# Performance work log

Measured on AMD Instinct MI355X. Metric: run time of the kernel, lower is better.

## Reference

```python
import jax, jax.numpy as jnp
import numpy as np

B, T_ENC, T_DEC = 32, 512, 32
ENC = DEC = EMB = ATT = OUT = 256
VOCAB = 32000
CHUNK = 8
SOS = 1


def _energy(enc, h, W, V, b, vv, g, vb, r):
    # enc: [B,T,ENC], h: [B,DEC] -> [B,T]
    t = jnp.tanh(enc @ W.T + (h @ V.T)[:, None, :] + b)           # [B,T,ATT]
    w_eff = (g[0] / jnp.linalg.norm(vv)) * vv                      # weight-normed v
    return t @ w_eff + vb[0] + r[0]


def _excl_cumprod(x):
    # exclusive safe cumprod along axis 1: [1, x0, x0*x1, ...]
    logs = jnp.cumsum(jnp.log(jnp.clip(x, 1e-10, 1.0)), axis=1)
    logs = jnp.concatenate([jnp.zeros_like(logs[:, :1]), logs[:, :-1]], axis=1)
    return jnp.exp(logs)


def _moving_sum(x, back, forward):
    # sliding-window sum over axis 1, window [j-back, j+forward]
    T = x.shape[1]
    w = back + forward + 1
    xp = jnp.pad(x, ((0, 0), (back, forward)))
    c = jnp.cumsum(xp, axis=1)
    c = jnp.concatenate([jnp.zeros_like(c[:, :1]), c], axis=1)
    return c[:, w:w + T] - c[:, :T]


def _chunkwise_beta(alpha, u, w):
    u = u - jnp.max(u, axis=1, keepdims=True)
    eu = jnp.exp(u)
    denom = jnp.clip(_moving_sum(eu, w - 1, 0), 1e-10, None)
    return eu * _moving_sum(alpha / denom, 0, w - 1)


def setup_inputs():
    key = jax.random.key(0)
    ks = jax.random.split(key, 20)
    s = 0.05
    rn = lambda k, shp: jax.random.normal(k, shp, jnp.float32) * s
    return {
        'encoder_outputs': jax.random.normal(ks[0], (B, T_ENC, ENC), jnp.float32),
        'decoder_inputs': jax.random.randint(ks[1], (B, T_DEC), 0, VOCAB),
        'h0': jax.random.normal(ks[2], (B, DEC), jnp.float32),
        'noise': jax.random.normal(ks[3], (T_DEC, B, T_ENC), jnp.float32),
        'emb': rn(ks[4], (VOCAB, EMB)),
        'W_ih': rn(ks[5], (DEC, EMB)), 'b_ih': jnp.zeros((DEC,), jnp.float32),
        'W_hh': rn(ks[6], (DEC, DEC)), 'b_hh': jnp.zeros((DEC,), jnp.float32),
        'Wm': rn(ks[7], (ATT, ENC)), 'Vm': rn(ks[8], (ATT, DEC)),
        'bm': rn(ks[9], (ATT,)), 'vvm': jax.random.normal(ks[10], (ATT,), jnp.float32),
        'gm': jnp.full((1,), (1.0 / ATT) ** 0.5, jnp.float32),
        'vbm': jnp.zeros((1,), jnp.float32), 'rm': jnp.full((1,), -4.0, jnp.float32),
        'Wc': rn(ks[11], (ATT, ENC)), 'Vc': rn(ks[12], (ATT, DEC)),
        'bc': rn(ks[13], (ATT,)), 'vvc': jax.random.normal(ks[14], (ATT,), jnp.float32),
        'gc': jnp.full((1,), (1.0 / ATT) ** 0.5, jnp.float32),
        'vbc': jnp.zeros((1,), jnp.float32), 'rc': jnp.full((1,), -4.0, jnp.float32),
        'W_comb': rn(ks[15], (OUT, ENC + DEC)),
        'W_proj': rn(ks[16], (VOCAB, OUT)), 'b_proj': jnp.zeros((VOCAB,), jnp.float32),
    }


def reference(encoder_outputs, decoder_inputs, h0, noise, emb,
              W_ih, b_ih, W_hh, b_hh,
              Wm, Vm, bm, vvm, gm, vbm, rm,
              Wc, Vc, bc, vvc, gc, vbc, rc,
              W_comb, W_proj, b_proj):
    batch = encoder_outputs.shape[0]
    alpha0 = jnp.zeros((batch, encoder_outputs.shape[1]), encoder_outputs.dtype).at[:, 0].set(1.0)
    x0 = jnp.full((batch,), SOS, dtype=decoder_inputs.dtype)

    def step(carry, xs):
        x_tok, h, alpha = carry
        noise_t, next_tok = xs
        x = emb[x_tok]                                             # embedding lookup
        h = jnp.tanh(x @ W_ih.T + b_ih + h @ W_hh.T + b_hh)        # RNNCell (tanh)
        e_m = _energy(encoder_outputs, h, Wm, Vm, bm, vvm, gm, vbm, rm)
        p = jax.nn.sigmoid(e_m + noise_t)
        cp = _excl_cumprod(1.0 - p)
        alpha = p * cp * jnp.cumsum(alpha / jnp.clip(cp, 1e-10, 1.0), axis=1)
        e_c = _energy(encoder_outputs, h, Wc, Vc, bc, vvc, gc, vbc, rc)
        beta = _chunkwise_beta(alpha, e_c, CHUNK)
        context = jnp.einsum('bt,bte->be', beta, encoder_outputs)
        attn = jnp.tanh(jnp.concatenate([context, h], axis=1) @ W_comb.T)
        logit = attn @ W_proj.T + b_proj
        return (next_tok, h, alpha), logit

    xs = (noise, decoder_inputs.T)
    _, logits = jax.lax.scan(step, (x0, h0, alpha0), xs)           # [T_dec,B,V]
    return jnp.transpose(logits, (1, 0, 2))                        # [B,T_dec,V]
```

## Files before the change

### kernel.cpp

```cpp
#include <hip/hip_runtime.h>
#include <cstddef>

#define B 32
#define T_ENC 512
#define T_DEC 32
#define E 256
#define VOCAB 32000
#define SOS 1

typedef __attribute__((ext_vector_type(8))) short short8;
typedef __attribute__((ext_vector_type(4))) float floatx4;

static const size_t OFF_ENCW   = 0;
static const size_t OFF_WEFFM  = OFF_ENCW + (size_t)B * T_ENC * 2 * E;
static const size_t OFF_WEFFC  = OFF_WEFFM + E;
static const size_t OFF_BSUM   = OFF_WEFFC + E;
static const size_t OFF_XIH    = OFF_BSUM + E;
static const size_t OFF_WHHT   = OFF_XIH + (size_t)T_DEC * B * E;
static const size_t OFF_VMT    = OFF_WHHT + (size_t)E * E;
static const size_t OFF_VCT    = OFF_VMT + (size_t)E * E;
static const size_t OFF_WCOMBT = OFF_VCT + (size_t)E * E;
static const size_t OFF_ATTNB  = OFF_WCOMBT + (size_t)2 * E * E;
static const size_t OFF_WPBF   = OFF_ATTNB + (size_t)T_DEC * B * E / 2;

static const size_t OUT_EMBX  = 0;
static const size_t OUT_BETA  = 262144;
static const size_t OUT_ACOMB = 786432;
static const size_t OUT_HALL  = 1310720;
static const size_t OUT_HV    = 1572864;
static const size_t OUT_PE    = 2097152;
static const size_t OUT_VMC   = 3145728;
static const size_t OUT_ZERO  = 3276800;
static const size_t OUT_WHI   = 3277312;
static const size_t OUT_WLO   = 3342848;
static const size_t OUT_B512  = 3408384;

__device__ __forceinline__ float ftanh(float x) {
  float ax = __builtin_fabsf(x);
  float e  = __expf(-2.f * ax);
  float r  = (1.f - e) * __builtin_amdgcn_rcpf(1.f + e);
  return __builtin_copysignf(r, x);
}

__device__ __forceinline__ float fsigmoid(float z) {
  return __builtin_amdgcn_rcpf(1.f + __expf(-z));
}

__device__ __forceinline__ float wredmax(float s) {
  s = fmaxf(s, __shfl_xor(s, 1, 64));  s = fmaxf(s, __shfl_xor(s, 2, 64));
  s = fmaxf(s, __shfl_xor(s, 4, 64));  s = fmaxf(s, __shfl_xor(s, 8, 64));
  s = fmaxf(s, __shfl_xor(s, 16, 64)); s = fmaxf(s, __shfl_xor(s, 32, 64));
  return s;
}

__device__ __forceinline__ unsigned short f2bf(float f) {
  unsigned int u = __float_as_uint(f);
  u = (u + 0x7fffu + ((u >> 16) & 1u)) >> 16;
  return (unsigned short)u;
}

__device__ __forceinline__ float bf2f(unsigned short h) {
  return __uint_as_float((unsigned int)h << 16);
}

__device__ __forceinline__ float wexcl(float tot, int lane) {
  float v = tot;
#pragma unroll
  for (int off = 1; off < 64; off <<= 1) {
    float y = __shfl_up(v, off, 64);
    if (lane >= off) v += y;
  }
  return v - tot;
}

__device__ __forceinline__ float dot4_wtanh(float4 s2a, float4 s2b, float4 w4) {
  float e, num, acc;
  e = __expf(s2a.x + s2b.x); num = __builtin_fmaf(-e, w4.x, w4.x);
  acc = num * __builtin_amdgcn_rcpf(1.f + e);
  e = __expf(s2a.y + s2b.y); num = __builtin_fmaf(-e, w4.y, w4.y);
  acc = __builtin_fmaf(num, __builtin_amdgcn_rcpf(1.f + e), acc);
  e = __expf(s2a.z + s2b.z); num = __builtin_fmaf(-e, w4.z, w4.z);
  acc = __builtin_fmaf(num, __builtin_amdgcn_rcpf(1.f + e), acc);
  e = __expf(s2a.w + s2b.w); num = __builtin_fmaf(-e, w4.w, w4.w);
  acc = __builtin_fmaf(num, __builtin_amdgcn_rcpf(1.f + e), acc);
  return acc;
}

__device__ __forceinline__ float4 scalem2(float4 v) {
  float4 r; r.x = -2.f * v.x; r.y = -2.f * v.y; r.z = -2.f * v.z; r.w = -2.f * v.w;
  return r;
}

__global__ __launch_bounds__(256) void prep_misc(
    const float* __restrict__ vvm, const float* __restrict__ gm, float* __restrict__ w_effm,
    const float* __restrict__ vvc, const float* __restrict__ gc, float* __restrict__ w_effc,
    const float* __restrict__ b_ih, const float* __restrict__ b_hh, float* __restrict__ bsum,
    const float* __restrict__ bm, const float* __restrict__ bc, float* __restrict__ bias512,
    const float* __restrict__ Vm, const float* __restrict__ Vc,
    float* __restrict__ Vmc, float* __restrict__ zero512,
    const float* __restrict__ Wm, const float* __restrict__ Wc,
    unsigned short* __restrict__ Whi, unsigned short* __restrict__ Wlo)
{
  __shared__ float red[256];
  const int blk = blockIdx.x, tid = threadIdx.x;
  if (blk < 2) {
    const float* vv = blk ? vvc : vvm;
    const float* g  = blk ? gc  : gm;
    float* out      = blk ? w_effc : w_effm;
    float v = vv[tid];
    red[tid] = v * v;
    __syncthreads();
    for (int off = 128; off > 0; off >>= 1) {
      if (tid < off) red[tid] += red[tid + off];
      __syncthreads();
    }
    float norm = sqrtf(red[0]);
    out[tid] = (g[0] / norm) * v;
  } else if (blk == 2) {
    bsum[tid] = b_ih[tid] + b_hh[tid];
    bias512[tid]       = bm[tid];
    bias512[256 + tid] = bc[tid];
    zero512[tid] = 0.f;
    zero512[256 + tid] = 0.f;
  } else if (blk < 131) {
    int i = (blk - 3) * 1024 + tid * 4;
    float4 v = (i < E * E) ? *(const float4*)(Vm + i) : *(const float4*)(Vc + i - E * E);
    *(float4*)(Vmc + i) = v;
  } else {
    int i = (blk - 131) * 1024 + tid * 4;
    float4 v = (i < E * E) ? *(const float4*)(Wm + i) : *(const float4*)(Wc + i - E * E);
    ushort4 h, l;
    h.x = f2bf(v.x); l.x = f2bf(v.x - bf2f(h.x));
    h.y = f2bf(v.y); l.y = f2bf(v.y - bf2f(h.y));
    h.z = f2bf(v.z); l.z = f2bf(v.z - bf2f(h.z));
    h.w = f2bf(v.w); l.w = f2bf(v.w - bf2f(h.w));
    *(ushort4*)(Whi + i) = h;
    *(ushort4*)(Wlo + i) = l;
  }
}

__global__ __launch_bounds__(256) void transpose2(
    const float* __restrict__ W_hh, float* __restrict__ W_hhT,
    const float* __restrict__ W_comb, float* __restrict__ W_combT)
{
  __shared__ float tl[32][33];
  const int blk = blockIdx.x;
  const float* in; float* out; int C, bx, by;
  if (blk < 64) { in = W_hh;   out = W_hhT;   C = 256; bx = blk & 7;  by = blk >> 3; }
  else { int k = blk - 64; in = W_comb; out = W_combT; C = 512; bx = k & 15; by = k >> 4; }
  const int R = 256;
  const int tx = threadIdx.x & 31, ty = threadIdx.x >> 5;
  const int c0 = bx * 32, r0 = by * 32;
#pragma unroll
  for (int k = 0; k < 4; k++)
    tl[ty + 8 * k][tx] = in[(size_t)(r0 + ty + 8 * k) * C + c0 + tx];
  __syncthreads();
#pragma unroll
  for (int k = 0; k < 4; k++)
    out[(size_t)(c0 + ty + 8 * k) * R + r0 + tx] = tl[tx][ty + 8 * k];
}

__global__ __launch_bounds__(256) void gather_emb(
    const int* __restrict__ dec, const float* __restrict__ emb, float* __restrict__ embX)
{
  int r = blockIdx.x, d = threadIdx.x;
  int s = r >> 5, b = r & 31;
  int tok = (s == 0) ? SOS : dec[b * T_DEC + s - 1];
  embX[(size_t)r * E + d] = emb[(size_t)tok * E + d];
}

__global__ __launch_bounds__(256) void cvt_bf16(
    const float* __restrict__ src, unsigned short* __restrict__ dst)
{
  size_t i = ((size_t)blockIdx.x * 256 + threadIdx.x) * 4;
  float4 v = *(const float4*)(src + i);
  ushort4 o;
  o.x = f2bf(v.x); o.y = f2bf(v.y); o.z = f2bf(v.z); o.w = f2bf(v.w);
  *(ushort4*)(dst + i) = o;
}

__global__ __launch_bounds__(256) void gemm_xwt(
    const float* __restrict__ A, const float* __restrict__ W,
    const float* __restrict__ bias, float* __restrict__ Y,
    int M, int N, int K)
{
  __shared__ float As[64][68];
  __shared__ float Ws[64][68];
  const int tid = threadIdx.x;
  const int tx = tid & 15, ty = tid >> 4;
  const int row0 = blockIdx.y * 64, col0 = blockIdx.x * 64;
  float acc[4][4];
#pragma unroll
  for (int i = 0; i < 4; i++)
#pragma unroll
    for (int j = 0; j < 4; j++) acc[i][j] = 0.f;

  for (int k0 = 0; k0 < K; k0 += 64) {
#pragma unroll
    for (int s = 0; s < 4; s++) {
      int i = (s << 4) + ty;
      int j = tx << 2;
      float4 av = *(const float4*)(A + (size_t)(row0 + i) * K + k0 + j);
      As[j][i] = av.x; As[j + 1][i] = av.y; As[j + 2][i] = av.z; As[j + 3][i] = av.w;
      float4 wv = *(const float4*)(W + (size_t)(col0 + i) * K + k0 + j);
      Ws[j][i] = wv.x; Ws[j + 1][i] = wv.y; Ws[j + 2][i] = wv.z; Ws[j + 3][i] = wv.w;
    }
    __syncthreads();
#pragma unroll
    for (int kk = 0; kk < 64; kk++) {
      const float4 af = *(const float4*)&As[kk][ty << 2];
      const float4 bf = *(const float4*)&Ws[kk][tx << 2];
      acc[0][0] += af.x * bf.x; acc[0][1] += af.x * bf.y; acc[0][2] += af.x * bf.z; acc[0][3] += af.x * bf.w;
      acc[1][0] += af.y * bf.x; acc[1][1] += af.y * bf.y; acc[1][2] += af.y * bf.z; acc[1][3] += af.y * bf.w;
      acc[2][0] += af.z * bf.x; acc[2][1] += af.z * bf.y; acc[2][2] += af.z * bf.z; acc[2][3] += af.z * bf.w;
      acc[3][0] += af.w * bf.x; acc[3][1] += af.w * bf.y; acc[3][2] += af.w * bf.z; acc[3][3] += af.w * bf.w;
    }
    __syncthreads();
  }
  const float4 bv = *(const float4*)(bias + col0 + (tx << 2));
#pragma unroll
  for (int i = 0; i < 4; i++) {
    float4 o;
    o.x = acc[i][0] + bv.x; o.y = acc[i][1] + bv.y;
    o.z = acc[i][2] + bv.z; o.w = acc[i][3] + bv.w;
    *(float4*)(Y + (size_t)(row0 + (ty << 2) + i) * N + col0 + (tx << 2)) = o;
  }
}

__global__ __launch_bounds__(256) void enc_mfma(
    const float* __restrict__ A,
    const unsigned short* __restrict__ Whi, const unsigned short* __restrict__ Wlo,
    const float* __restrict__ bias512, float* __restrict__ Y)
{
  __shared__ unsigned short a_hi[64][264];
  __shared__ unsigned short a_lo[64][264];
  const int tid = threadIdx.x;
  const int row0 = blockIdx.x * 64;
#pragma unroll
  for (int u = 0; u < 16; ++u) {
    int f = tid + (u << 8);
    int r = f >> 6, c = (f & 63) << 2;
    float4 v = *(const float4*)(A + (size_t)(row0 + r) * E + c);
    ushort4 h, l;
    h.x = f2bf(v.x); l.x = f2bf(v.x - bf2f(h.x));
    h.y = f2bf(v.y); l.y = f2bf(v.y - bf2f(h.y));
    h.z = f2bf(v.z); l.z = f2bf(v.z - bf2f(h.z));
    h.w = f2bf(v.w); l.w = f2bf(v.w - bf2f(h.w));
    *(ushort4*)&a_hi[r][c] = h;
    *(ushort4*)&a_lo[r][c] = l;
  }
  __syncthreads();
  const int lane = tid & 63, w = tid >> 6;
  const int m = lane & 15, q = lane >> 4;
  const int colbase = w << 7;
#pragma unroll
  for (int cp = 0; cp < 4; ++cp) {
    const int c0 = colbase + (cp << 5);
    floatx4 acc[4][2] = {};
    for (int k0 = 0; k0 < E; k0 += 32) {
      const size_t w0 = (size_t)(c0 + m) * E + (q << 3) + k0;
      const size_t w1 = (size_t)(c0 + 16 + m) * E + (q << 3) + k0;
      short8 bh0 = *(const short8*)(Whi + w0);
      short8 bl0 = *(const short8*)(Wlo + w0);
      short8 bh1 = *(const short8*)(Whi + w1);
      short8 bl1 = *(const short8*)(Wlo + w1);
#pragma unroll
      for (int rg = 0; rg < 4; ++rg) {
        short8 ah = *(const short8*)&a_hi[(rg << 4) + m][(q << 3) + k0];
        short8 al = *(const short8*)&a_lo[(rg << 4) + m][(q << 3) + k0];
        acc[rg][0] = __builtin_amdgcn_mfma_f32_16x16x32_bf16(ah, bh0, acc[rg][0], 0, 0, 0);
        acc[rg][0] = __builtin_amdgcn_mfma_f32_16x16x32_bf16(al, bh0, acc[rg][0], 0, 0, 0);
        acc[rg][0] = __builtin_amdgcn_mfma_f32_16x16x32_bf16(ah, bl0, acc[rg][0], 0, 0, 0);
        acc[rg][0] = __builtin_amdgcn_mfma_f32_16x16x32_bf16(al, bl0, acc[rg][0], 0, 0, 0);
        acc[rg][1] = __builtin_amdgcn_mfma_f32_16x16x32_bf16(ah, bh1, acc[rg][1], 0, 0, 0);
        acc[rg][1] = __builtin_amdgcn_mfma_f32_16x16x32_bf16(al, bh1, acc[rg][1], 0, 0, 0);
        acc[rg][1] = __builtin_amdgcn_mfma_f32_16x16x32_bf16(ah, bl1, acc[rg][1], 0, 0, 0);
        acc[rg][1] = __builtin_amdgcn_mfma_f32_16x16x32_bf16(al, bl1, acc[rg][1], 0, 0, 0);
      }
    }
    const float bia0 = bias512[c0 + m], bia1 = bias512[c0 + 16 + m];
#pragma unroll
    for (int rg = 0; rg < 4; ++rg)
#pragma unroll
      for (int r = 0; r < 4; ++r) {
        const size_t row = row0 + (rg << 4) + (q << 2) + r;
        Y[row * (2 * E) + c0 + m]      = acc[rg][0][r] + bia0;
        Y[row * (2 * E) + c0 + 16 + m] = acc[rg][1][r] + bia1;
      }
  }
}

__global__ __launch_bounds__(1024) void hchain_kernel(
    const float* __restrict__ Xih, const float* __restrict__ W_hhT,
    const float* __restrict__ h0,
    float* __restrict__ A_comb, float* __restrict__ h_all)
{
  __shared__ float h_s[E];
  __shared__ float red[1024];
  const int b = blockIdx.x, tid = threadIdx.x;
  const int c = tid >> 8, d = tid & 255, k0 = c * 64;
  float wreg[64];
#pragma unroll
  for (int j = 0; j < 64; ++j) wreg[j] = W_hhT[(size_t)(k0 + j) * E + d];
  if (tid < E) h_s[tid] = h0[(size_t)b * E + tid];
  __syncthreads();
  for (int s = 0; s < T_DEC; ++s) {
    float acc = 0.f;
#pragma unroll
    for (int j = 0; j < 64; j += 4) {
      float4 hh = *(const float4*)&h_s[k0 + j];
      acc += hh.x * wreg[j] + hh.y * wreg[j + 1] + hh.z * wreg[j + 2] + hh.w * wreg[j + 3];
    }
    red[tid] = acc;
    __syncthreads();
    if (tid < E) {
      float v = red[tid] + red[256 + tid] + red[512 + tid] + red[768 + tid]
              + Xih[((size_t)s * B + b) * E + tid];
      float hh = ftanh(v);
      h_s[tid] = hh;
      A_comb[((size_t)(b * T_DEC + s)) * (2 * E) + E + tid] = hh;
      h_all[((size_t)(b * T_DEC + s)) * E + tid] = hh;
    }
    __syncthreads();
  }
}

__global__ __launch_bounds__(512) void energy_kernel(
    const float* __restrict__ encW, const float* __restrict__ g_hv,
    const float* __restrict__ w_effm, const float* __restrict__ w_effc,
    const float* __restrict__ vbm, const float* __restrict__ rmp,
    const float* __restrict__ vbc, const float* __restrict__ rcp_,
    float* __restrict__ g_pe)
{
  __shared__ float hv_s[16 * 512];
  const int b = blockIdx.x, t0 = blockIdx.y << 5, s0 = blockIdx.z << 4;
  const int tid = threadIdx.x, lane = tid & 63, w = tid >> 6;
  const float* hvb = g_hv + ((size_t)(b * T_DEC + s0)) * 512;
  for (int i = tid * 4; i < 16 * 512; i += 2048) {
    float4 v = *(const float4*)(hvb + i);
    *(float4*)&hv_s[i] = scalem2(v);
  }
  __syncthreads();

  const float embias = vbm[0] + rmp[0];
  const float ecbias = vbc[0] + rcp_[0];
  const float bias_l = ((lane >> 2) & 1) ? ecbias : embias;
  const float4 wm4 = *(const float4*)(w_effm + lane * 4);
  const float4 wc4 = *(const float4*)(w_effc + lane * 4);
  const int t = t0 + (w << 2);
  const size_t rb = ((size_t)(b * T_ENC + t)) * 512 + lane * 4;
  const float4 em0 = scalem2(*(const float4*)(encW + rb));
  const float4 em1 = scalem2(*(const float4*)(encW + rb + 512));
  const float4 em2 = scalem2(*(const float4*)(encW + rb + 1024));
  const float4 em3 = scalem2(*(const float4*)(encW + rb + 1536));
  const float4 ec0 = scalem2(*(const float4*)(encW + rb + 256));
  const float4 ec1 = scalem2(*(const float4*)(encW + rb + 768));
  const float4 ec2 = scalem2(*(const float4*)(encW + rb + 1280));
  const float4 ec3 = scalem2(*(const float4*)(encW + rb + 1792));

  const bool sb0 = lane & 1, sb1 = lane & 2, sb2 = lane & 4;
  const int myr = lane >> 3;
  float pv0 = 0.f, pv1 = 0.f;

  for (int sl = 0; sl < 16; ++sl) {
    const float4 hm4 = *(const float4*)&hv_s[(sl << 9) + lane * 4];
    const float4 hc4 = *(const float4*)&hv_s[(sl << 9) + 256 + lane * 4];
    float v0 = dot4_wtanh(em0, hm4, wm4);
    float v1 = dot4_wtanh(em1, hm4, wm4);
    float v2 = dot4_wtanh(em2, hm4, wm4);
    float v3 = dot4_wtanh(em3, hm4, wm4);
    float v4 = dot4_wtanh(ec0, hc4, wc4);
    float v5 = dot4_wtanh(ec1, hc4, wc4);
    float v6 = dot4_wtanh(ec2, hc4, wc4);
    float v7 = dot4_wtanh(ec3, hc4, wc4);
    float k0_ = sb0 ? v1 : v0, s0_ = sb0 ? v0 : v1; k0_ += __shfl_xor(s0_, 1, 64);
    float k1_ = sb0 ? v3 : v2, s1_ = sb0 ? v2 : v3; k1_ += __shfl_xor(s1_, 1, 64);
    float k2_ = sb0 ? v5 : v4, s2_ = sb0 ? v4 : v5; k2_ += __shfl_xor(s2_, 1, 64);
    float k3_ = sb0 ? v7 : v6, s3_ = sb0 ? v6 : v7; k3_ += __shfl_xor(s3_, 1, 64);
    float kA = sb1 ? k1_ : k0_, sA = sb1 ? k0_ : k1_; kA += __shfl_xor(sA, 2, 64);
    float kB = sb1 ? k3_ : k2_, sB = sb1 ? k2_ : k3_; kB += __shfl_xor(sB, 2, 64);
    float dd = sb2 ? kB : kA, sD = sb2 ? kA : kB; dd += __shfl_xor(sD, 4, 64);
    dd += __shfl_xor(dd, 8, 64);
    dd += __shfl_xor(dd, 16, 64);
    dd += __shfl_xor(dd, 32, 64);
    float val = dd + bias_l;
    if ((sl & 7) == myr) {
      if (sl & 8) pv1 = val; else pv0 = val;
    }
  }
  const int row_l = lane & 3, type = (lane >> 2) & 1;
  const int tS = t + row_l;
  const int col = type * 32 + s0 + myr;
  g_pe[((size_t)((b << 6) + col)) * 512 + tS]     = pv0;
  g_pe[((size_t)((b << 6) + col + 8)) * 512 + tS] = pv1;
}

__global__ __launch_bounds__(64) void scan_kernel(
    const float* __restrict__ g_pe, const float* __restrict__ noise,
    float* __restrict__ beta_all)
{
  const int b = blockIdx.x, lane = threadIdx.x;
  const float* pe = g_pe + ((size_t)b << 15);
  float alpha[8];
#pragma unroll
  for (int i = 0; i < 8; ++i) alpha[i] = 0.f;
  if (lane == 0) alpha[0] = 1.f;

  for (int s = 0; s < T_DEC; ++s) {
    const float* nrow = noise + ((size_t)s * B + b) * T_ENC + lane * 8;
    float4 n0 = *(const float4*)nrow;
    float4 n1 = *(const float4*)(nrow + 4);
    float nz[8] = {n0.x, n0.y, n0.z, n0.w, n1.x, n1.y, n1.z, n1.w};
    const float* psm = pe + (size_t)s * 512 + lane * 8;
    const float* pec = pe + (size_t)(32 + s) * 512 + lane * 8;
    float4 m0 = *(const float4*)psm;
    float4 m1 = *(const float4*)(psm + 4);
    float4 e0 = *(const float4*)pec;
    float4 e1 = *(const float4*)(pec + 4);
    float smv[8] = {m0.x, m0.y, m0.z, m0.w, m1.x, m1.y, m1.z, m1.w};
    float ec[8]  = {e0.x, e0.y, e0.z, e0.w, e1.x, e1.y, e1.z, e1.w};
    float p[8];
#pragma unroll
    for (int i = 0; i < 8; ++i) p[i] = fsigmoid(smv[i] + nz[i]);
    float lgv[8], lci[8], run = 0.f;
#pragma unroll
    for (int i = 0; i < 8; ++i) {
      float omp = fminf(fmaxf(1.f - p[i], 1e-10f), 1.f);
      lgv[i] = __logf(omp);
      run += lgv[i];
      lci[i] = run;
    }
    float ex1 = wexcl(run, lane);
    float cp[8], ao[8];
#pragma unroll
    for (int i = 0; i < 8; ++i) {
      float incl = lci[i] + ex1;
      cp[i] = __expf(incl - lgv[i]);
      float cpc = fminf(fmaxf(cp[i], 1e-10f), 1.f);
      ao[i] = alpha[i] * __builtin_amdgcn_rcpf(cpc);
    }
    float run2 = 0.f, lc2[8];
#pragma unroll
    for (int i = 0; i < 8; ++i) { run2 += ao[i]; lc2[i] = run2; }
    float ex2 = wexcl(run2, lane);
    float alpha_new[8];
#pragma unroll
    for (int i = 0; i < 8; ++i) alpha_new[i] = p[i] * cp[i] * (lc2[i] + ex2);
    float mloc = ec[0];
#pragma unroll
    for (int i = 1; i < 8; ++i) mloc = fmaxf(mloc, ec[i]);
    float mx = wredmax(mloc);
    float eu[8];
#pragma unroll
    for (int i = 0; i < 8; ++i) eu[i] = __expf(ec[i] - mx);
    float run3 = 0.f, c1[8];
#pragma unroll
    for (int i = 0; i < 8; ++i) { run3 += eu[i]; c1[i] = run3; }
    float ex3 = wexcl(run3, lane);
#pragma unroll
    for (int i = 0; i < 8; ++i) c1[i] += ex3;
    float r[8];
#pragma unroll
    for (int i = 0; i < 8; ++i) {
      float up = __shfl_up(c1[i], 1, 64);
      float prev = (lane == 0) ? 0.f : up;
      float denom = fmaxf(c1[i] - prev, 1e-10f);
      r[i] = alpha_new[i] * __builtin_amdgcn_rcpf(denom);
    }
    float run4 = 0.f, c2[8];
#pragma unroll
    for (int i = 0; i < 8; ++i) { run4 += r[i]; c2[i] = run4; }
    float ex4 = wexcl(run4, lane);
#pragma unroll
    for (int i = 0; i < 8; ++i) c2[i] += ex4;
    float c2_7 = c2[7];
    float dn[8];
#pragma unroll
    for (int i = 0; i < 8; ++i) dn[i] = __shfl_down(c2[i], 1, 64);
    float up7 = __shfl_up(c2_7, 1, 64);
    float beta[8];
#pragma unroll
    for (int i = 0; i < 8; ++i) {
      float hi = (i == 0) ? c2_7 : ((lane == 63) ? c2_7 : dn[i - 1]);
      float lo = (i == 0) ? ((lane == 0) ? 0.f : up7) : c2[i - 1];
      beta[i] = eu[i] * (hi - lo);
    }
    float* bp = beta_all + ((size_t)(b * T_DEC + s)) * T_ENC + lane * 8;
    *(float4*)bp       = (float4){beta[0], beta[1], beta[2], beta[3]};
    *(float4*)(bp + 4) = (float4){beta[4], beta[5], beta[6], beta[7]};
#pragma unroll
    for (int i = 0; i < 8; ++i) alpha[i] = alpha_new[i];
  }
}

__global__ __launch_bounds__(256) void context_kernel(
    const float* __restrict__ beta_all, const float* __restrict__ enc,
    float* __restrict__ A_comb)
{
  __shared__ float smem[T_ENC * 36];
  const int b = blockIdx.x, e0 = blockIdx.y << 6;
  const int tid = threadIdx.x;
  const float* bp = beta_all + (size_t)b * T_DEC * T_ENC;
  for (int i = tid; i < T_DEC * T_ENC; i += 256) {
    int s2 = i >> 9, t = i & 511;
    smem[t * 36 + s2] = bp[i];
  }
  __syncthreads();
  const int el = tid & 63, tg = tid >> 6;
  float4 a8[8];
#pragma unroll
  for (int u = 0; u < 8; ++u) a8[u] = (float4){0.f, 0.f, 0.f, 0.f};
  const float* ep = enc + (size_t)b * T_ENC * E + e0 + el;
  for (int t = tg; t < T_ENC; t += 4) {
    float v = ep[(size_t)t * E];
    const float4* bt = (const float4*)&smem[t * 36];
#pragma unroll
    for (int u = 0; u < 8; ++u) {
      float4 bv = bt[u];
      a8[u].x += bv.x * v; a8[u].y += bv.y * v;
      a8[u].z += bv.z * v; a8[u].w += bv.w * v;
    }
  }
  __syncthreads();
#pragma unroll
  for (int u = 0; u < 8; ++u) {
    smem[((tg * T_DEC + u * 4 + 0) << 6) + el] = a8[u].x;
    smem[((tg * T_DEC + u * 4 + 1) << 6) + el] = a8[u].y;
    smem[((tg * T_DEC + u * 4 + 2) << 6) + el] = a8[u].z;
    smem[((tg * T_DEC + u * 4 + 3) << 6) + el] = a8[u].w;
  }
  __syncthreads();
  for (int o = tid; o < T_DEC * 64; o += 256) {
    int s2 = o >> 6, e = o & 63;
    float v = smem[(s2 << 6) + e] + smem[((T_DEC + s2) << 6) + e]
            + smem[((2 * T_DEC + s2) << 6) + e] + smem[((3 * T_DEC + s2) << 6) + e];
    A_comb[((size_t)(b * T_DEC + s2)) * (2 * E) + e0 + e] = v;
  }
}

__global__ __launch_bounds__(256) void comb_tanh_kernel(
    const float* __restrict__ A, const float* __restrict__ Wt,
    unsigned short* __restrict__ attn_bf)
{
  __shared__ float As[64][68];
  __shared__ float Ws[64][68];
  const int tid = threadIdx.x, tx = tid & 15, ty = tid >> 4;
  const int row0 = blockIdx.y * 64, col0 = blockIdx.x * 64;
  float acc[4][4];
#pragma unroll
  for (int i = 0; i < 4; i++)
#pragma unroll
    for (int jj = 0; jj < 4; jj++) acc[i][jj] = 0.f;

  for (int k0 = 0; k0 < 2 * E; k0 += 64) {
#pragma unroll
    for (int ss = 0; ss < 4; ss++) {
      int i = (ss << 4) + ty;
      int jj = tx << 2;
      float4 av = *(const float4*)(A + (size_t)(row0 + i) * (2 * E) + k0 + jj);
      As[jj][i] = av.x; As[jj + 1][i] = av.y; As[jj + 2][i] = av.z; As[jj + 3][i] = av.w;
      float4 wv = *(const float4*)(Wt + (size_t)(k0 + i) * E + col0 + jj);
      *(float4*)&Ws[i][jj] = wv;
    }
    __syncthreads();
#pragma unroll
    for (int kk = 0; kk < 64; kk++) {
      const float4 af = *(const float4*)&As[kk][ty << 2];
      const float4 bf = *(const float4*)&Ws[kk][tx << 2];
      acc[0][0] += af.x * bf.x; acc[0][1] += af.x * bf.y; acc[0][2] += af.x * bf.z; acc[0][3] += af.x * bf.w;
      acc[1][0] += af.y * bf.x; acc[1][1] += af.y * bf.y; acc[1][2] += af.y * bf.z; acc[1][3] += af.y * bf.w;
      acc[2][0] += af.z * bf.x; acc[2][1] += af.z * bf.y; acc[2][2] += af.z * bf.z; acc[2][3] += af.z * bf.w;
      acc[3][0] += af.w * bf.x; acc[3][1] += af.w * bf.y; acc[3][2] += af.w * bf.z; acc[3][3] += af.w * bf.w;
    }
    __syncthreads();
  }
#pragma unroll
  for (int i = 0; i < 4; i++) {
    ushort4 o;
    o.x = f2bf(ftanh(acc[i][0])); o.y = f2bf(ftanh(acc[i][1]));
    o.z = f2bf(ftanh(acc[i][2])); o.w = f2bf(ftanh(acc[i][3]));
    *(ushort4*)(attn_bf + (size_t)(row0 + (ty << 2) + i) * E + col0 + (tx << 2)) = o;
  }
}

__global__ __launch_bounds__(256) void proj_mfma(
    const unsigned short* __restrict__ A, const unsigned short* __restrict__ Bw,
    const float* __restrict__ bias, float* __restrict__ Y)
{
  __shared__ unsigned short wl[64][264];
  __shared__ float tile[64][68];
  const int tid = threadIdx.x;
  const int wave = tid >> 6, lane = tid & 63;
  const int m = lane & 15, q = lane >> 4;
  const int col0 = blockIdx.x * 64;
#pragma unroll
  for (int u = 0; u < 16; ++u) {
    int f = tid + (u << 8);
    int r = f >> 6, c = (f & 63) << 2;
    *(ushort4*)&wl[r][c] = *(const ushort4*)(Bw + (size_t)(col0 + r) * E + c);
  }
  __syncthreads();

  for (int mt = 0; mt < 16; ++mt) {
    const int rowa = mt * 64 + wave * 16;
    floatx4 acc0 = {0.f, 0.f, 0.f, 0.f}, acc1 = acc0, acc2 = acc0, acc3 = acc0;
    const unsigned short* ar = A + (size_t)(rowa + m) * E + q * 8;
#pragma unroll
    for (int k0 = 0; k0 < E; k0 += 32) {
      short8 af = *(const short8*)(ar + k0);
      short8 b0 = *(const short8*)&wl[ 0 + m][q * 8 + k0];
      short8 b1 = *(const short8*)&wl[16 + m][q * 8 + k0];
      short8 b2 = *(const short8*)&wl[32 + m][q * 8 + k0];
      short8 b3 = *(const short8*)&wl[48 + m][q * 8 + k0];
      acc0 = __builtin_amdgcn_mfma_f32_16x16x32_bf16(af, b0, acc0, 0, 0, 0);
      acc1 = __builtin_amdgcn_mfma_f32_16x16x32_bf16(af, b1, acc1, 0, 0, 0);
      acc2 = __builtin_amdgcn_mfma_f32_16x16x32_bf16(af, b2, acc2, 0, 0, 0);
      acc3 = __builtin_amdgcn_mfma_f32_16x16x32_bf16(af, b3, acc3, 0, 0, 0);
    }
    const int rl = wave * 16 + q * 4;
#pragma unroll
    for (int r = 0; r < 4; r++) {
      tile[rl + r][ 0 + m] = acc0[r];
      tile[rl + r][16 + m] = acc1[r];
      tile[rl + r][32 + m] = acc2[r];
      tile[rl + r][48 + m] = acc3[r];
    }
    __syncthreads();
    const int row = tid >> 2, seg = tid & 3;
    const size_t yb = ((size_t)mt * 64 + row) * VOCAB + col0;
#pragma unroll
    for (int u = 0; u < 4; u++) {
      int cc = seg * 16 + u * 4;
      float4 v = *(const float4*)&tile[row][cc];
      float4 bb = *(const float4*)(bias + col0 + cc);
      v.x += bb.x; v.y += bb.y; v.z += bb.z; v.w += bb.w;
      *(float4*)(Y + yb + cc) = v;
    }
    __syncthreads();
  }
}

extern "C" void kernel_launch(void* const* d_in, const int* in_sizes, int n_in,
                              void* d_out, int out_size, void* d_ws, size_t ws_size,
                              hipStream_t stream)
{
  (void)in_sizes; (void)n_in; (void)out_size; (void)ws_size;
  const float* enc    = (const float*)d_in[0];
  const int*   dec    = (const int*)d_in[1];
  const float* h0     = (const float*)d_in[2];
  const float* noise  = (const float*)d_in[3];
  const float* emb    = (const float*)d_in[4];
  const float* W_ih   = (const float*)d_in[5];
  const float* b_ih   = (const float*)d_in[6];
  const float* W_hh   = (const float*)d_in[7];
  const float* b_hh   = (const float*)d_in[8];
  const float* Wm     = (const float*)d_in[9];
  const float* Vm     = (const float*)d_in[10];
  const float* bm     = (const float*)d_in[11];
  const float* vvm    = (const float*)d_in[12];
  const float* gm     = (const float*)d_in[13];
  const float* vbm    = (const float*)d_in[14];
  const float* rmp    = (const float*)d_in[15];
  const float* Wc     = (const float*)d_in[16];
  const float* Vc     = (const float*)d_in[17];
  const float* bc     = (const float*)d_in[18];
  const float* vvc    = (const float*)d_in[19];
  const float* gc     = (const float*)d_in[20];
  const float* vbc    = (const float*)d_in[21];
  const float* rcp_   = (const float*)d_in[22];
  const float* W_comb = (const float*)d_in[23];
  const float* W_proj = (const float*)d_in[24];
  const float* b_proj = (const float*)d_in[25];

  float* ws = (float*)d_ws;
  float* encW    = ws + OFF_ENCW;
  float* w_effm  = ws + OFF_WEFFM;
  float* w_effc  = ws + OFF_WEFFC;
  float* bsum    = ws + OFF_BSUM;
  float* Xih     = ws + OFF_XIH;
  float* W_hhT   = ws + OFF_WHHT;
  float* W_combT = ws + OFF_WCOMBT;
  unsigned short* attn_bf = (unsigned short*)(ws + OFF_ATTNB);
  unsigned short* Wp_bf   = (unsigned short*)(ws + OFF_WPBF);

  float* outF = (float*)d_out;
  float* embX     = outF + OUT_EMBX;
  float* beta_all = outF + OUT_BETA;
  float* A_comb   = outF + OUT_ACOMB;
  float* h_all    = outF + OUT_HALL;
  float* g_hv     = outF + OUT_HV;
  float* g_pe     = outF + OUT_PE;
  float* Vmc      = outF + OUT_VMC;
  float* zero512  = outF + OUT_ZERO;
  unsigned short* Whi = (unsigned short*)(outF + OUT_WHI);
  unsigned short* Wlo = (unsigned short*)(outF + OUT_WLO);
  float* bias512  = outF + OUT_B512;

  prep_misc<<<259, 256, 0, stream>>>(vvm, gm, w_effm, vvc, gc, w_effc,
                                     b_ih, b_hh, bsum, bm, bc, bias512,
                                     Vm, Vc, Vmc, zero512, Wm, Wc, Whi, Wlo);
  transpose2<<<192, 256, 0, stream>>>(W_hh, W_hhT, W_comb, W_combT);
  gather_emb<<<T_DEC * B, 256, 0, stream>>>(dec, emb, embX);
  gemm_xwt<<<dim3(E / 64, (T_DEC * B) / 64), 256, 0, stream>>>(embX, W_ih, bsum, Xih,
                                                               T_DEC * B, E, E);
  enc_mfma<<<(B * T_ENC) / 64, 256, 0, stream>>>(enc, Whi, Wlo, bias512, encW);
  cvt_bf16<<<(VOCAB * E) / 1024, 256, 0, stream>>>(W_proj, Wp_bf);

  hchain_kernel<<<B, 1024, 0, stream>>>(Xih, W_hhT, h0, A_comb, h_all);

  gemm_xwt<<<dim3((2 * E) / 64, (T_DEC * B) / 64), 256, 0, stream>>>(
      h_all, Vmc, zero512, g_hv, T_DEC * B, 2 * E, E);

  energy_kernel<<<dim3(B, 16, 2), 512, 0, stream>>>(
      encW, g_hv, w_effm, w_effc, vbm, rmp, vbc, rcp_, g_pe);

  scan_kernel<<<B, 64, 0, stream>>>(g_pe, noise, beta_all);

  context_kernel<<<dim3(B, 4), 256, 0, stream>>>(beta_all, enc, A_comb);
  comb_tanh_kernel<<<dim3(E / 64, (T_DEC * B) / 64), 256, 0, stream>>>(A_comb, W_combT, attn_bf);
  proj_mfma<<<VOCAB / 64, 256, 0, stream>>>(attn_bf, Wp_bf, b_proj, outF);
}
```

Before: 580.1 us.

## Fuse prep kernels, overlap RNN chain with encoder GEMM, split projection blocks

Merges the weight preparation, transposes, embedding gather and bf16 conversion into one launch, and runs the serial RNN hidden-state chain in the same launch as the encoder projection GEMM so the two overlap. The tanh energy uses exp2 with a prescaled constant, the scan reorders the softmax-max work to interleave with the cumprod, and the vocabulary projection uses twice as many blocks. These cut launch count and idle time on the serial chain. The cost is larger 1024-thread encoder blocks with higher shared memory use, and the reloaded weight tiles per projection block are now shared by fewer rows.

```diff
diff --git a/kernel.cpp b/kernel.cpp
--- a/kernel.cpp
+++ b/kernel.cpp
@@ -7,6 +7,7 @@
 #define E 256
 #define VOCAB 32000
 #define SOS 1
+#define NEG2LOG2E -2.885390081777927f
 
 typedef __attribute__((ext_vector_type(8))) short short8;
 typedef __attribute__((ext_vector_type(4))) float floatx4;
@@ -75,23 +76,25 @@
 
 __device__ __forceinline__ float dot4_wtanh(float4 s2a, float4 s2b, float4 w4) {
   float e, num, acc;
-  e = __expf(s2a.x + s2b.x); num = __builtin_fmaf(-e, w4.x, w4.x);
+  e = __builtin_exp2f(s2a.x + s2b.x); num = __builtin_fmaf(-e, w4.x, w4.x);
   acc = num * __builtin_amdgcn_rcpf(1.f + e);
-  e = __expf(s2a.y + s2b.y); num = __builtin_fmaf(-e, w4.y, w4.y);
+  e = __builtin_exp2f(s2a.y + s2b.y); num = __builtin_fmaf(-e, w4.y, w4.y);
   acc = __builtin_fmaf(num, __builtin_amdgcn_rcpf(1.f + e), acc);
-  e = __expf(s2a.z + s2b.z); num = __builtin_fmaf(-e, w4.z, w4.z);
+  e = __builtin_exp2f(s2a.z + s2b.z); num = __builtin_fmaf(-e, w4.z, w4.z);
   acc = __builtin_fmaf(num, __builtin_amdgcn_rcpf(1.f + e), acc);
-  e = __expf(s2a.w + s2b.w); num = __builtin_fmaf(-e, w4.w, w4.w);
+  e = __builtin_exp2f(s2a.w + s2b.w); num = __builtin_fmaf(-e, w4.w, w4.w);
   acc = __builtin_fmaf(num, __builtin_amdgcn_rcpf(1.f + e), acc);
   return acc;
 }
 
 __device__ __forceinline__ float4 scalem2(float4 v) {
-  float4 r; r.x = -2.f * v.x; r.y = -2.f * v.y; r.z = -2.f * v.z; r.w = -2.f * v.w;
+  float4 r;
+  r.x = NEG2LOG2E * v.x; r.y = NEG2LOG2E * v.y;
+  r.z = NEG2LOG2E * v.z; r.w = NEG2LOG2E * v.w;
   return r;
 }
 
-__global__ __launch_bounds__(256) void prep_misc(
+__global__ __launch_bounds__(256) void prep_all(
     const float* __restrict__ vvm, const float* __restrict__ gm, float* __restrict__ w_effm,
     const float* __restrict__ vvc, const float* __restrict__ gc, float* __restrict__ w_effc,
     const float* __restrict__ b_ih, const float* __restrict__ b_hh, float* __restrict__ bsum,
@@ -99,9 +102,14 @@
     const float* __restrict__ Vm, const float* __restrict__ Vc,
     float* __restrict__ Vmc, float* __restrict__ zero512,
     const float* __restrict__ Wm, const float* __restrict__ Wc,
-    unsigned short* __restrict__ Whi, unsigned short* __restrict__ Wlo)
+    unsigned short* __restrict__ Whi, unsigned short* __restrict__ Wlo,
+    const float* __restrict__ W_hh, float* __restrict__ W_hhT,
+    const float* __restrict__ W_comb, float* __restrict__ W_combT,
+    const int* __restrict__ dec, const float* __restrict__ emb, float* __restrict__ embX,
+    const float* __restrict__ W_proj, unsigned short* __restrict__ Wp_bf)
 {
   __shared__ float red[256];
+  __shared__ float tl[32][33];
   const int blk = blockIdx.x, tid = threadIdx.x;
   if (blk < 2) {
     const float* vv = blk ? vvc : vvm;
@@ -126,7 +134,7 @@
     int i = (blk - 3) * 1024 + tid * 4;
     float4 v = (i < E * E) ? *(const float4*)(Vm + i) : *(const float4*)(Vc + i - E * E);
     *(float4*)(Vmc + i) = v;
-  } else {
+  } else if (blk < 259) {
     int i = (blk - 131) * 1024 + tid * 4;
     float4 v = (i < E * E) ? *(const float4*)(Wm + i) : *(const float4*)(Wc + i - E * E);
     ushort4 h, l;
@@ -136,47 +144,33 @@
     h.w = f2bf(v.w); l.w = f2bf(v.w - bf2f(h.w));
     *(ushort4*)(Whi + i) = h;
     *(ushort4*)(Wlo + i) = l;
-  }
-}
-
-__global__ __launch_bounds__(256) void transpose2(
-    const float* __restrict__ W_hh, float* __restrict__ W_hhT,
-    const float* __restrict__ W_comb, float* __restrict__ W_combT)
-{
-  __shared__ float tl[32][33];
-  const int blk = blockIdx.x;
-  const float* in; float* out; int C, bx, by;
-  if (blk < 64) { in = W_hh;   out = W_hhT;   C = 256; bx = blk & 7;  by = blk >> 3; }
-  else { int k = blk - 64; in = W_comb; out = W_combT; C = 512; bx = k & 15; by = k >> 4; }
-  const int R = 256;
-  const int tx = threadIdx.x & 31, ty = threadIdx.x >> 5;
-  const int c0 = bx * 32, r0 = by * 32;
-#pragma unroll
-  for (int k = 0; k < 4; k++)
-    tl[ty + 8 * k][tx] = in[(size_t)(r0 + ty + 8 * k) * C + c0 + tx];
-  __syncthreads();
-#pragma unroll
-  for (int k = 0; k < 4; k++)
-    out[(size_t)(c0 + ty + 8 * k) * R + r0 + tx] = tl[tx][ty + 8 * k];
-}
-
-__global__ __launch_bounds__(256) void gather_emb(
-    const int* __restrict__ dec, const float* __restrict__ emb, float* __restrict__ embX)
-{
-  int r = blockIdx.x, d = threadIdx.x;
-  int s = r >> 5, b = r & 31;
-  int tok = (s == 0) ? SOS : dec[b * T_DEC + s - 1];
-  embX[(size_t)r * E + d] = emb[(size_t)tok * E + d];
-}
-
-__global__ __launch_bounds__(256) void cvt_bf16(
-    const float* __restrict__ src, unsigned short* __restrict__ dst)
-{
-  size_t i = ((size_t)blockIdx.x * 256 + threadIdx.x) * 4;
-  float4 v = *(const float4*)(src + i);
-  ushort4 o;
-  o.x = f2bf(v.x); o.y = f2bf(v.y); o.z = f2bf(v.z); o.w = f2bf(v.w);
-  *(ushort4*)(dst + i) = o;
+  } else if (blk < 451) {
+    int k2 = blk - 259;
+    const float* in; float* out; int C, bx, by;
+    if (k2 < 64) { in = W_hh;   out = W_hhT;   C = 256; bx = k2 & 7;  by = k2 >> 3; }
+    else { int k = k2 - 64; in = W_comb; out = W_combT; C = 512; bx = k & 15; by = k >> 4; }
+    const int R = 256;
+    const int tx = tid & 31, ty = tid >> 5;
+    const int c0 = bx * 32, r0 = by * 32;
+#pragma unroll
+    for (int k = 0; k < 4; k++)
+      tl[ty + 8 * k][tx] = in[(size_t)(r0 + ty + 8 * k) * C + c0 + tx];
+    __syncthreads();
+#pragma unroll
+    for (int k = 0; k < 4; k++)
+      out[(size_t)(c0 + ty + 8 * k) * R + r0 + tx] = tl[tx][ty + 8 * k];
+  } else if (blk < 1475) {
+    int r = blk - 451;
+    int s = r >> 5, b = r & 31;
+    int tok = (s == 0) ? SOS : dec[b * T_DEC + s - 1];
+    embX[(size_t)r * E + tid] = emb[(size_t)tok * E + tid];
+  } else {
+    size_t i = ((size_t)(blk - 1475) * 256 + tid) * 4;
+    float4 v = *(const float4*)(W_proj + i);
+    ushort4 o;
+    o.x = f2bf(v.x); o.y = f2bf(v.y); o.z = f2bf(v.z); o.w = f2bf(v.w);
+    *(ushort4*)(Wp_bf + i) = o;
+  }
 }
 
 __global__ __launch_bounds__(256) void gemm_xwt(
@@ -227,35 +221,67 @@
   }
 }
 
-__global__ __launch_bounds__(256) void enc_mfma(
-    const float* __restrict__ A,
+__global__ __launch_bounds__(1024, 1) void hchain_enc(
+    const float* __restrict__ Xih, const float* __restrict__ W_hhT,
+    const float* __restrict__ h0,
+    float* __restrict__ A_comb, float* __restrict__ h_all,
+    const float* __restrict__ encA,
     const unsigned short* __restrict__ Whi, const unsigned short* __restrict__ Wlo,
-    const float* __restrict__ bias512, float* __restrict__ Y)
-{
-  __shared__ unsigned short a_hi[64][264];
-  __shared__ unsigned short a_lo[64][264];
+    const float* __restrict__ bias512, float* __restrict__ encW)
+{
+  __shared__ __align__(16) unsigned char smem_raw[67584];
   const int tid = threadIdx.x;
-  const int row0 = blockIdx.x * 64;
-#pragma unroll
-  for (int u = 0; u < 16; ++u) {
-    int f = tid + (u << 8);
-    int r = f >> 6, c = (f & 63) << 2;
-    float4 v = *(const float4*)(A + (size_t)(row0 + r) * E + c);
-    ushort4 h, l;
-    h.x = f2bf(v.x); l.x = f2bf(v.x - bf2f(h.x));
-    h.y = f2bf(v.y); l.y = f2bf(v.y - bf2f(h.y));
-    h.z = f2bf(v.z); l.z = f2bf(v.z - bf2f(h.z));
-    h.w = f2bf(v.w); l.w = f2bf(v.w - bf2f(h.w));
-    *(ushort4*)&a_hi[r][c] = h;
-    *(ushort4*)&a_lo[r][c] = l;
-  }
-  __syncthreads();
-  const int lane = tid & 63, w = tid >> 6;
-  const int m = lane & 15, q = lane >> 4;
-  const int colbase = w << 7;
-#pragma unroll
-  for (int cp = 0; cp < 4; ++cp) {
-    const int c0 = colbase + (cp << 5);
+
+  if (blockIdx.x < B) {
+    float* h_s = (float*)smem_raw;
+    float* red = h_s + 256;
+    const int b = blockIdx.x;
+    const int c = tid >> 8, d = tid & 255, k0 = c * 64;
+    float wreg[64];
+#pragma unroll
+    for (int j = 0; j < 64; ++j) wreg[j] = W_hhT[(size_t)(k0 + j) * E + d];
+    if (tid < E) h_s[tid] = h0[(size_t)b * E + tid];
+    __syncthreads();
+    for (int s = 0; s < T_DEC; ++s) {
+      float acc = 0.f;
+#pragma unroll
+      for (int j = 0; j < 64; j += 4) {
+        float4 hh = *(const float4*)&h_s[k0 + j];
+        acc += hh.x * wreg[j] + hh.y * wreg[j + 1] + hh.z * wreg[j + 2] + hh.w * wreg[j + 3];
+      }
+      red[tid] = acc;
+      __syncthreads();
+      if (tid < E) {
+        float v = red[tid] + red[256 + tid] + red[512 + tid] + red[768 + tid]
+                + Xih[((size_t)s * B + b) * E + tid];
+        float hh = ftanh(v);
+        h_s[tid] = hh;
+        A_comb[((size_t)(b * T_DEC + s)) * (2 * E) + E + tid] = hh;
+        h_all[((size_t)(b * T_DEC + s)) * E + tid] = hh;
+      }
+      __syncthreads();
+    }
+  } else {
+    unsigned short* a_hi = (unsigned short*)smem_raw;
+    unsigned short* a_lo = a_hi + 64 * 264;
+    const int row0 = (int)(blockIdx.x - B) * 64;
+#pragma unroll
+    for (int u = 0; u < 4; ++u) {
+      int f = tid + (u << 10);
+      int r = f >> 6, cc = (f & 63) << 2;
+      float4 v = *(const float4*)(encA + (size_t)(row0 + r) * E + cc);
+      ushort4 h, l;
+      h.x = f2bf(v.x); l.x = f2bf(v.x - bf2f(h.x));
+      h.y = f2bf(v.y); l.y = f2bf(v.y - bf2f(h.y));
+      h.z = f2bf(v.z); l.z = f2bf(v.z - bf2f(h.z));
+      h.w = f2bf(v.w); l.w = f2bf(v.w - bf2f(h.w));
+      *(ushort4*)&a_hi[r * 264 + cc] = h;
+      *(ushort4*)&a_lo[r * 264 + cc] = l;
+    }
+    __syncthreads();
+    const int lane = tid & 63, w = tid >> 6;
+    const int m = lane & 15, q = lane >> 4;
+    const int c0 = w << 5;
     floatx4 acc[4][2] = {};
     for (int k0 = 0; k0 < E; k0 += 32) {
       const size_t w0 = (size_t)(c0 + m) * E + (q << 3) + k0;
@@ -266,8 +292,8 @@
       short8 bl1 = *(const short8*)(Wlo + w1);
 #pragma unroll
       for (int rg = 0; rg < 4; ++rg) {
-        short8 ah = *(const short8*)&a_hi[(rg << 4) + m][(q << 3) + k0];
-        short8 al = *(const short8*)&a_lo[(rg << 4) + m][(q << 3) + k0];
+        short8 ah = *(const short8*)&a_hi[((rg << 4) + m) * 264 + (q << 3) + k0];
+        short8 al = *(const short8*)&a_lo[((rg << 4) + m) * 264 + (q << 3) + k0];
         acc[rg][0] = __builtin_amdgcn_mfma_f32_16x16x32_bf16(ah, bh0, acc[rg][0], 0, 0, 0);
         acc[rg][0] = __builtin_amdgcn_mfma_f32_16x16x32_bf16(al, bh0, acc[rg][0], 0, 0, 0);
         acc[rg][0] = __builtin_amdgcn_mfma_f32_16x16x32_bf16(ah, bl0, acc[rg][0], 0, 0, 0);
@@ -284,44 +310,9 @@
 #pragma unroll
       for (int r = 0; r < 4; ++r) {
         const size_t row = row0 + (rg << 4) + (q << 2) + r;
-        Y[row * (2 * E) + c0 + m]      = acc[rg][0][r] + bia0;
-        Y[row * (2 * E) + c0 + 16 + m] = acc[rg][1][r] + bia1;
+        encW[row * (2 * E) + c0 + m]      = acc[rg][0][r] + bia0;
+        encW[row * (2 * E) + c0 + 16 + m] = acc[rg][1][r] + bia1;
       }
-  }
-}
-
-__global__ __launch_bounds__(1024) void hchain_kernel(
-    const float* __restrict__ Xih, const float* __restrict__ W_hhT,
-    const float* __restrict__ h0,
-    float* __restrict__ A_comb, float* __restrict__ h_all)
-{
-  __shared__ float h_s[E];
-  __shared__ float red[1024];
-  const int b = blockIdx.x, tid = threadIdx.x;
-  const int c = tid >> 8, d = tid & 255, k0 = c * 64;
-  float wreg[64];
-#pragma unroll
-  for (int j = 0; j < 64; ++j) wreg[j] = W_hhT[(size_t)(k0 + j) * E + d];
-  if (tid < E) h_s[tid] = h0[(size_t)b * E + tid];
-  __syncthreads();
-  for (int s = 0; s < T_DEC; ++s) {
-    float acc = 0.f;
-#pragma unroll
-    for (int j = 0; j < 64; j += 4) {
-      float4 hh = *(const float4*)&h_s[k0 + j];
-      acc += hh.x * wreg[j] + hh.y * wreg[j + 1] + hh.z * wreg[j + 2] + hh.w * wreg[j + 3];
-    }
-    red[tid] = acc;
-    __syncthreads();
-    if (tid < E) {
-      float v = red[tid] + red[256 + tid] + red[512 + tid] + red[768 + tid]
-              + Xih[((size_t)s * B + b) * E + tid];
-      float hh = ftanh(v);
-      h_s[tid] = hh;
-      A_comb[((size_t)(b * T_DEC + s)) * (2 * E) + E + tid] = hh;
-      h_all[((size_t)(b * T_DEC + s)) * E + tid] = hh;
-    }
-    __syncthreads();
   }
 }
 
@@ -430,35 +421,34 @@
       run += lgv[i];
       lci[i] = run;
     }
+    float mloc = ec[0];
+#pragma unroll
+    for (int i = 1; i < 8; ++i) mloc = fmaxf(mloc, ec[i]);
     float ex1 = wexcl(run, lane);
-    float cp[8], ao[8];
+    float mx  = wredmax(mloc);
+    float cp[8], ao[8], eu[8];
 #pragma unroll
     for (int i = 0; i < 8; ++i) {
       float incl = lci[i] + ex1;
       cp[i] = __expf(incl - lgv[i]);
       float cpc = fminf(fmaxf(cp[i], 1e-10f), 1.f);
       ao[i] = alpha[i] * __builtin_amdgcn_rcpf(cpc);
-    }
-    float run2 = 0.f, lc2[8];
-#pragma unroll
-    for (int i = 0; i < 8; ++i) { run2 += ao[i]; lc2[i] = run2; }
+      eu[i] = __expf(ec[i] - mx);
+    }
+    float run2 = 0.f, lc2[8], run3 = 0.f, c1[8];
+#pragma unroll
+    for (int i = 0; i < 8; ++i) {
+      run2 += ao[i]; lc2[i] = run2;
+      run3 += eu[i]; c1[i] = run3;
+    }
     float ex2 = wexcl(run2, lane);
+    float ex3 = wexcl(run3, lane);
     float alpha_new[8];
 #pragma unroll
-    for (int i = 0; i < 8; ++i) alpha_new[i] = p[i] * cp[i] * (lc2[i] + ex2);
-    float mloc = ec[0];
-#pragma unroll
-    for (int i = 1; i < 8; ++i) mloc = fmaxf(mloc, ec[i]);
-    float mx = wredmax(mloc);
-    float eu[8];
-#pragma unroll
-    for (int i = 0; i < 8; ++i) eu[i] = __expf(ec[i] - mx);
-    float run3 = 0.f, c1[8];
-#pragma unroll
-    for (int i = 0; i < 8; ++i) { run3 += eu[i]; c1[i] = run3; }
-    float ex3 = wexcl(run3, lane);
-#pragma unroll
-    for (int i = 0; i < 8; ++i) c1[i] += ex3;
+    for (int i = 0; i < 8; ++i) {
+      alpha_new[i] = p[i] * cp[i] * (lc2[i] + ex2);
+      c1[i] += ex3;
+    }
     float r[8];
 #pragma unroll
     for (int i = 0; i < 8; ++i) {
@@ -592,7 +582,8 @@
   const int tid = threadIdx.x;
   const int wave = tid >> 6, lane = tid & 63;
   const int m = lane & 15, q = lane >> 4;
-  const int col0 = blockIdx.x * 64;
+  const int col0 = (blockIdx.x >> 1) * 64;
+  const int mt0 = (blockIdx.x & 1) * 8;
 #pragma unroll
   for (int u = 0; u < 16; ++u) {
     int f = tid + (u << 8);
@@ -601,7 +592,7 @@
   }
   __syncthreads();
 
-  for (int mt = 0; mt < 16; ++mt) {
+  for (int mt = mt0; mt < mt0 + 8; ++mt) {
     const int rowa = mt * 64 + wave * 16;
     floatx4 acc0 = {0.f, 0.f, 0.f, 0.f}, acc1 = acc0, acc2 = acc0, acc3 = acc0;
     const unsigned short* ar = A + (size_t)(rowa + m) * E + q * 8;
@@ -696,27 +687,21 @@
   unsigned short* Wlo = (unsigned short*)(outF + OUT_WLO);
   float* bias512  = outF + OUT_B512;
 
-  prep_misc<<<259, 256, 0, stream>>>(vvm, gm, w_effm, vvc, gc, w_effc,
+  prep_all<<<9475, 256, 0, stream>>>(vvm, gm, w_effm, vvc, gc, w_effc,
                                      b_ih, b_hh, bsum, bm, bc, bias512,
-                                     Vm, Vc, Vmc, zero512, Wm, Wc, Whi, Wlo);
-  transpose2<<<192, 256, 0, stream>>>(W_hh, W_hhT, W_comb, W_combT);
-  gather_emb<<<T_DEC * B, 256, 0, stream>>>(dec, emb, embX);
+                                     Vm, Vc, Vmc, zero512, Wm, Wc, Whi, Wlo,
+                                     W_hh, W_hhT, W_comb, W_combT,
+                                     dec, emb, embX, W_proj, Wp_bf);
   gemm_xwt<<<dim3(E / 64, (T_DEC * B) / 64), 256, 0, stream>>>(embX, W_ih, bsum, Xih,
                                                                T_DEC * B, E, E);
-  enc_mfma<<<(B * T_ENC) / 64, 256, 0, stream>>>(enc, Whi, Wlo, bias512, encW);
-  cvt_bf16<<<(VOCAB * E) / 1024, 256, 0, stream>>>(W_proj, Wp_bf);
-
-  hchain_kernel<<<B, 1024, 0, stream>>>(Xih, W_hhT, h0, A_comb, h_all);
-
+  hchain_enc<<<B + (B * T_ENC) / 64, 1024, 0, stream>>>(
+      Xih, W_hhT, h0, A_comb, h_all, enc, Whi, Wlo, bias512, encW);
   gemm_xwt<<<dim3((2 * E) / 64, (T_DEC * B) / 64), 256, 0, stream>>>(
       h_all, Vmc, zero512, g_hv, T_DEC * B, 2 * E, E);
-
   energy_kernel<<<dim3(B, 16, 2), 512, 0, stream>>>(
       encW, g_hv, w_effm, w_effc, vbm, rmp, vbc, rcp_, g_pe);
-
   scan_kernel<<<B, 64, 0, stream>>>(g_pe, noise, beta_all);
-
   context_kernel<<<dim3(B, 4), 256, 0, stream>>>(beta_all, enc, A_comb);
   comb_tanh_kernel<<<dim3(E / 64, (T_DEC * B) / 64), 256, 0, stream>>>(A_comb, W_combT, attn_bf);
-  proj_mfma<<<VOCAB / 64, 256, 0, stream>>>(attn_bf, Wp_bf, b_proj, outF);
-}
+  proj_mfma<<<2 * (VOCAB / 64), 256, 0, stream>>>(attn_bf, Wp_bf, b_proj, outF);
+}
```

After: 580.0 us. No clear change (-0.0%).
